# Kernel tuning notes

Hardware: AMD Instinct MI355X
Metric: run time of the kernel (lower is better)

Reference implementation:

```python
import jax, jax.numpy as jnp
import numpy as np

NEG_SLOPE = 0.2   # GATConv default leaky_relu slope
BN_EPS = 1e-5
N, D, H, DH, E, BS = 49152, 512, 8, 64, 131072, 12
N_LAYERS = 5  # conv6 exists in __init__ but is never called in forward


def setup_inputs() -> dict:
    key = jax.random.key(0)
    ks = jax.random.split(key, 12)
    s = 0.05
    x = jax.random.normal(ks[0], (N, D), jnp.float32)
    edge_index = jax.random.randint(ks[1], (2, E), 0, N, jnp.int64)
    Ws = jax.random.normal(ks[2], (N_LAYERS, D, H * DH), jnp.float32) * s
    Asrc = jax.random.normal(ks[3], (N_LAYERS, H, DH), jnp.float32) * s
    Adst = jax.random.normal(ks[4], (N_LAYERS, H, DH), jnp.float32) * s
    Bconv = jax.random.normal(ks[5], (N_LAYERS, H * DH), jnp.float32) * s
    Gamma = jnp.ones((N_LAYERS, D), jnp.float32)
    Beta = jnp.zeros((N_LAYERS, D), jnp.float32)
    Wl = jax.random.normal(ks[6], (D, 1), jnp.float32) * s
    bl = jnp.zeros((1,), jnp.float32)
    return {"x": x, "edge_index": edge_index, "Ws": Ws, "Asrc": Asrc,
            "Adst": Adst, "Bconv": Bconv, "Gamma": Gamma, "Beta": Beta,
            "Wl": Wl, "bl": bl, "bs": BS}


def _gat_conv(x, src, dst, W, a_src, a_dst, b):
    n = x.shape[0]
    h = (x @ W).reshape(n, H, DH)                      # [N,H,DH]
    al_s = jnp.einsum('nhd,hd->nh', h, a_src)          # [N,H]
    al_d = jnp.einsum('nhd,hd->nh', h, a_dst)
    e = jax.nn.leaky_relu(al_s[src] + al_d[dst], NEG_SLOPE)  # [Etot,H]
    # segment softmax over incoming edges of each dst node
    m = jax.ops.segment_max(e, dst, num_segments=n)
    p = jnp.exp(e - m[dst])
    z = jax.ops.segment_sum(p, dst, num_segments=n)
    alpha = p / (z[dst] + 1e-16)
    out = jax.ops.segment_sum(alpha[:, :, None] * h[src], dst, num_segments=n)
    return out.reshape(n, H * DH) + b


def _batch_norm(x, gamma, beta):
    mu = x.mean(0)
    var = x.var(0)  # biased, as torch BN uses for normalization
    return (x - mu) * jax.lax.rsqrt(var + BN_EPS) * gamma + beta


def reference(x, edge_index, Ws, Asrc, Adst, Bconv, Gamma, Beta, Wl, bl, bs):
    n = x.shape[0]
    loops = jnp.arange(n, dtype=edge_index.dtype)      # add_self_loops=True
    src = jnp.concatenate([edge_index[0], loops])
    dst = jnp.concatenate([edge_index[1], loops])
    for i in range(N_LAYERS):
        x = _gat_conv(x, src, dst, Ws[i], Asrc[i], Adst[i], Bconv[i])
        x = jax.nn.relu(_batch_norm(x, Gamma[i], Beta[i]))
    w = x @ Wl + bl                                    # [N,1]
    return w.reshape(bs, -1)
```

## Files before the change

kernel.cpp:

```cpp
#include <hip/hip_runtime.h>
#include <cstdint>

#define N_NODES 49152
#define DIM 512
#define NH 8
#define DHEAD 64
#define NE 131072
#define ETOT (NE + N_NODES)
#define NLAYERS 5
#define AGG_NODES 32
#define AGG_BLOCKS (N_NODES / AGG_NODES)

typedef short short8 __attribute__((ext_vector_type(8)));
typedef float floatx4 __attribute__((ext_vector_type(4)));

__device__ __forceinline__ float bf2f(unsigned short v) {
  union { unsigned int u; float f; } x; x.u = ((unsigned int)v) << 16; return x.f;
}
__device__ __forceinline__ unsigned short f2bf(float f) {
  union { float f; unsigned int u; } x; x.f = f;
  unsigned int r = x.u + 0x7fffu + ((x.u >> 16) & 1u);
  return (unsigned short)(r >> 16);
}
__device__ __forceinline__ void async_load16(const void* g, void* l) {
  __builtin_amdgcn_global_load_lds((const __attribute__((address_space(1))) void*)g,
                                   (__attribute__((address_space(3))) void*)l, 16, 0, 0);
}

__global__ __launch_bounds__(256) void convert_x_r10(const float* __restrict__ xf, unsigned short* __restrict__ xb)
{
  const size_t i = ((size_t)blockIdx.x * 256 + threadIdx.x) * 8;
  const float4 a = *(const float4*)&xf[i];
  const float4 b = *(const float4*)&xf[i + 4];
  unsigned int ov[4];
  ov[0] = (unsigned int)f2bf(a.x) | ((unsigned int)f2bf(a.y) << 16);
  ov[1] = (unsigned int)f2bf(a.z) | ((unsigned int)f2bf(a.w) << 16);
  ov[2] = (unsigned int)f2bf(b.x) | ((unsigned int)f2bf(b.y) << 16);
  ov[3] = (unsigned int)f2bf(b.z) | ((unsigned int)f2bf(b.w) << 16);
  *(uint4*)&xb[i] = *(const uint4*)ov;
}

__global__ void transpose_w_r10(const float* __restrict__ Ws, unsigned short* __restrict__ WT)
{
  __shared__ float tile[32][33];
  const int l  = blockIdx.z;
  const int nt = blockIdx.x * 32, kt = blockIdx.y * 32;
  const int tx = threadIdx.x & 31, ty = threadIdx.x >> 5;
  #pragma unroll
  for (int r = 0; r < 32; r += 8)
    tile[ty + r][tx] = Ws[(size_t)l*DIM*DIM + (size_t)(kt + ty + r)*DIM + nt + tx];
  __syncthreads();
  #pragma unroll
  for (int r = 0; r < 32; r += 8)
    WT[(size_t)l*DIM*DIM + (size_t)(nt + ty + r)*DIM + kt + tx] = f2bf(tile[tx][ty + r]);
}

__global__ void repack_edges_r10(const int* __restrict__ raw, int* __restrict__ eidx)
{
  const int i = blockIdx.x * 256 + threadIdx.x;
  bool is64 = true;
  #pragma unroll
  for (int j = 0; j < 16; j++) is64 = is64 && (raw[2*j + 1] == 0);
  int v;
  if (is64) v = (int)((const long long*)raw)[i];
  else      v = raw[i];
  eidx[i] = v;
}

__global__ void init_counts_r10(int* __restrict__ counts) {
  counts[blockIdx.x * 256 + threadIdx.x] = 1;
}
__global__ void hist_dst_r10(const int* __restrict__ eidx, int* __restrict__ counts) {
  const int i = blockIdx.x * 256 + threadIdx.x;
  atomicAdd(&counts[eidx[NE + i]], 1);
}
__global__ void scan_kernel_r10(const int* __restrict__ counts, int* __restrict__ offs, int* __restrict__ cursor)
{
  __shared__ int tot[1024];
  const int t = threadIdx.x;
  const int base = t * 48;
  int s = 0;
  for (int i = 0; i < 48; i++) s += counts[base + i];
  tot[t] = s;
  __syncthreads();
  for (int o = 1; o < 1024; o <<= 1) {
    int v = (t >= o) ? tot[t - o] : 0;
    __syncthreads();
    tot[t] += v;
    __syncthreads();
  }
  int run = tot[t] - s;
  for (int i = 0; i < 48; i++) {
    offs[base + i] = run;
    cursor[base + i] = run;
    run += counts[base + i];
  }
  if (t == 1023) offs[N_NODES] = tot[1023];
}
__global__ void scatter_edges_r10(const int* __restrict__ eidx, int* __restrict__ cursor, int* __restrict__ csrc)
{
  const int i = blockIdx.x * 256 + threadIdx.x;
  int s, d;
  if (i < NE) { s = eidx[i]; d = eidx[NE + i]; }
  else        { s = i - NE; d = s; }
  const int pos = atomicAdd(&cursor[d], 1);
  csrc[pos] = s;
}

__global__ __launch_bounds__(512, 4) void gemm_bt_r10(const unsigned short* __restrict__ A,
                                                      const unsigned short* __restrict__ BT,
                                                      const float* __restrict__ asrc,
                                                      const float* __restrict__ adst,
                                                      const float* __restrict__ bnscale,
                                                      const float* __restrict__ bnshift,
                                                      unsigned short* __restrict__ C,
                                                      float* __restrict__ als,
                                                      float* __restrict__ ald)
{
  __shared__ unsigned short As[128 * 64];
  __shared__ unsigned short Bs[256 * 64];
  const int m0 = blockIdx.x * 128;
  const int n0 = blockIdx.y * 256;
  const int tid = threadIdx.x;
  const int wv = tid >> 6, lane = tid & 63;
  const int wr = (wv & 1) * 64, wc = (wv >> 1) * 64;
  const int q = lane >> 4, c16 = lane & 15;
  const int arow = lane >> 3;
  const int acol = (lane & 7) * 8;
  const int sr = tid >> 3;
  const int sk = (tid & 7) * 8;

  floatx4 acc[4][4] = {};

  for (int k0 = 0; k0 < DIM; k0 += 64) {
    #pragma unroll
    for (int t = 0; t < 4; t++) {
      const int cb = wv * 4 + t;
      async_load16(BT + (size_t)(n0 + cb*8 + arow)*DIM + k0 + acol, &Bs[cb * 512]);
    }
    if (bnscale) {
      const uint4 x0 = *(const uint4*)&A[(size_t)(m0 + sr)      * DIM + k0 + sk];
      const uint4 x1 = *(const uint4*)&A[(size_t)(m0 + sr + 64) * DIM + k0 + sk];
      const float4 sc0 = *(const float4*)&bnscale[k0 + sk];
      const float4 sc1 = *(const float4*)&bnscale[k0 + sk + 4];
      const float4 sh0 = *(const float4*)&bnshift[k0 + sk];
      const float4 sh1 = *(const float4*)&bnshift[k0 + sk + 4];
      const float scv[8] = {sc0.x, sc0.y, sc0.z, sc0.w, sc1.x, sc1.y, sc1.z, sc1.w};
      const float shv[8] = {sh0.x, sh0.y, sh0.z, sh0.w, sh1.x, sh1.y, sh1.z, sh1.w};
      const uint4 xs[2] = {x0, x1};
      #pragma unroll
      for (int t = 0; t < 2; t++) {
        const unsigned int* xp = (const unsigned int*)&xs[t];
        unsigned int ov[4];
        #pragma unroll
        for (int j = 0; j < 4; j++) {
          const float a = bf2f((unsigned short)(xp[j] & 0xffffu));
          const float b = bf2f((unsigned short)(xp[j] >> 16));
          const float ya = fmaxf(0.f, a * scv[2*j]     + shv[2*j]);
          const float yb = fmaxf(0.f, b * scv[2*j + 1] + shv[2*j + 1]);
          ov[j] = (unsigned int)f2bf(ya) | ((unsigned int)f2bf(yb) << 16);
        }
        *(uint4*)&As[(sr + t*64) * 64 + sk] = *(const uint4*)ov;
      }
    } else {
      #pragma unroll
      for (int t = 0; t < 2; t++) {
        const int cb = wv * 2 + t;
        async_load16(A + (size_t)(m0 + cb*8 + arow)*DIM + k0 + acol, &As[cb * 512]);
      }
    }
    __syncthreads();
    #pragma unroll
    for (int kk = 0; kk < 64; kk += 32) {
      short8 aF[4], bF[4];
      #pragma unroll
      for (int mt = 0; mt < 4; mt++)
        aF[mt] = *(const short8*)&As[(wr + mt*16 + c16) * 64 + kk + q*8];
      #pragma unroll
      for (int nt = 0; nt < 4; nt++)
        bF[nt] = *(const short8*)&Bs[(wc + nt*16 + c16) * 64 + kk + q*8];
      #pragma unroll
      for (int mt = 0; mt < 4; mt++)
        #pragma unroll
        for (int nt = 0; nt < 4; nt++)
          acc[mt][nt] = __builtin_amdgcn_mfma_f32_16x16x32_bf16(aF[mt], bF[nt], acc[mt][nt], 0, 0, 0);
    }
    __syncthreads();
  }
  #pragma unroll
  for (int mt = 0; mt < 4; mt++) {
    #pragma unroll
    for (int nt = 0; nt < 4; nt++) {
      const int col = n0 + wc + nt*16 + c16;
      #pragma unroll
      for (int r = 0; r < 4; r++) {
        const int row = m0 + wr + mt*16 + q*4 + r;
        C[(size_t)row * DIM + col] = f2bf(acc[mt][nt][r]);
      }
    }
  }
  const int head = 4 * blockIdx.y + (wc >> 6);
  float as_[4], ad_[4];
  #pragma unroll
  for (int nt = 0; nt < 4; nt++) {
    const int d = nt * 16 + c16;
    as_[nt] = asrc[head * DHEAD + d];
    ad_[nt] = adst[head * DHEAD + d];
  }
  #pragma unroll
  for (int mt = 0; mt < 4; mt++) {
    #pragma unroll
    for (int r = 0; r < 4; r++) {
      float ss = 0.f, sd = 0.f;
      #pragma unroll
      for (int nt = 0; nt < 4; nt++) {
        ss += acc[mt][nt][r] * as_[nt];
        sd += acc[mt][nt][r] * ad_[nt];
      }
      #pragma unroll
      for (int msk = 1; msk <= 8; msk <<= 1) {
        ss += __shfl_xor(ss, msk, 64);
        sd += __shfl_xor(sd, msk, 64);
      }
      if (c16 == 0) {
        const int row = m0 + wr + mt*16 + q*4 + r;
        als[row * NH + head] = ss;
        ald[row * NH + head] = sd;
      }
    }
  }
}

__global__ __launch_bounds__(512, 4) void gat_agg_r10(const unsigned short* __restrict__ Hm,
    const float* __restrict__ als, const float* __restrict__ ald,
    const int* __restrict__ offs, const int* __restrict__ csrc,
    const float* __restrict__ bconv, unsigned short* __restrict__ Xout,
    float* __restrict__ ps, float* __restrict__ pq)
{
  __shared__ float red[8][1024];
  const int wv = threadIdx.x >> 6, lane = threadIdx.x & 63;
  const int hd = lane >> 3;
  const int hp = lane & 7;
  const int slot = lane >> 3;
  const float4 bA = ((const float4*)(bconv + (size_t)lane * 8))[0];
  const float4 bB = ((const float4*)(bconv + (size_t)lane * 8))[1];
  const float barr[8] = {bA.x, bA.y, bA.z, bA.w, bB.x, bB.y, bB.z, bB.w};
  float cs[8] = {}, cq[8] = {};

  #pragma unroll 1
  for (int i = 0; i < 4; i++) {
    const int node = blockIdx.x * AGG_NODES + wv * 4 + i;
    const int e0 = offs[node], e1 = offs[node + 1];
    const int deg = e1 - e0;
    float acc[8] = {};
    float zinv;

    if (deg <= 8) {
      const float aldp = ald[node * NH + hp];
      const int myS = csrc[e0 + ((lane < deg) ? lane : 0)];
      const int s_slot = __shfl(myS, slot, 64);
      float lg = als[s_slot * NH + hp] + aldp;
      lg = lg > 0.f ? lg : 0.2f * lg;
      const float lgv = (slot < deg) ? lg : -1e30f;
      float mx = fmaxf(lgv, __shfl_xor(lgv, 8, 64));
      mx = fmaxf(mx, __shfl_xor(mx, 16, 64));
      mx = fmaxf(mx, __shfl_xor(mx, 32, 64));
      const float w = __expf(lgv - mx);
      float z = w + __shfl_xor(w, 8, 64);
      z += __shfl_xor(z, 16, 64);
      z += __shfl_xor(z, 32, 64);
      zinv = 1.f / (__shfl(z, hd, 64) + 1e-16f);

      #pragma unroll
      for (int g = 0; g < 2; g++) {
        const int b = g * 4;
        if (b < deg) {
          const int k1 = (b+1 < deg) ? b+1 : 0;
          const int k2 = (b+2 < deg) ? b+2 : 0;
          const int k3 = (b+3 < deg) ? b+3 : 0;
          const int s0 = __shfl(myS, b,  64);
          const int s1 = __shfl(myS, k1, 64);
          const int s2 = __shfl(myS, k2, 64);
          const int s3 = __shfl(myS, k3, 64);
          const uint4 h0v = *(const uint4*)&Hm[(size_t)s0 * DIM + lane * 8];
          const uint4 h1v = *(const uint4*)&Hm[(size_t)s1 * DIM + lane * 8];
          const uint4 h2v = *(const uint4*)&Hm[(size_t)s2 * DIM + lane * 8];
          const uint4 h3v = *(const uint4*)&Hm[(size_t)s3 * DIM + lane * 8];
          const float w0 = __shfl(w, (b+0)*8 + hd, 64);
          const float w1 = __shfl(w, (b+1)*8 + hd, 64);
          const float w2 = __shfl(w, (b+2)*8 + hd, 64);
          const float w3 = __shfl(w, (b+3)*8 + hd, 64);
          const unsigned int* p0 = (const unsigned int*)&h0v;
          const unsigned int* p1 = (const unsigned int*)&h1v;
          const unsigned int* p2 = (const unsigned int*)&h2v;
          const unsigned int* p3 = (const unsigned int*)&h3v;
          #pragma unroll
          for (int j = 0; j < 4; j++) {
            acc[2*j]   += w0 * bf2f((unsigned short)(p0[j] & 0xffffu))
                        + w1 * bf2f((unsigned short)(p1[j] & 0xffffu))
                        + w2 * bf2f((unsigned short)(p2[j] & 0xffffu))
                        + w3 * bf2f((unsigned short)(p3[j] & 0xffffu));
            acc[2*j+1] += w0 * bf2f((unsigned short)(p0[j] >> 16))
                        + w1 * bf2f((unsigned short)(p1[j] >> 16))
                        + w2 * bf2f((unsigned short)(p2[j] >> 16))
                        + w3 * bf2f((unsigned short)(p3[j] >> 16));
          }
        }
      }
    } else if (deg <= 64) {
      const float aldp = ald[node * NH + hp];
      const int myS = (lane < deg) ? csrc[e0 + lane] : 0;
      const int nr = (deg + 7) >> 3;
      float lgsto[8];
      #pragma unroll
      for (int r = 0; r < 8; r++) {
        if (r < nr) {
          const int k = r * 8 + slot;
          const int s = __shfl(myS, k & 63, 64);
          float lg = als[s * NH + hp] + aldp;
          lg = lg > 0.f ? lg : 0.2f * lg;
          lgsto[r] = (k < deg) ? lg : -1e30f;
        } else lgsto[r] = -1e30f;
      }
      float m = lgsto[0];
      #pragma unroll
      for (int r = 1; r < 8; r++) m = fmaxf(m, lgsto[r]);
      m = fmaxf(m, __shfl_xor(m, 8, 64));
      m = fmaxf(m, __shfl_xor(m, 16, 64));
      m = fmaxf(m, __shfl_xor(m, 32, 64));
      float z = 0.f;
      float wsto[8];
      #pragma unroll
      for (int r = 0; r < 8; r++) {
        if (r < nr) {
          const float w = __expf(lgsto[r] - m);
          wsto[r] = w; z += w;
        } else wsto[r] = 0.f;
      }
      z += __shfl_xor(z, 8, 64);
      z += __shfl_xor(z, 16, 64);
      z += __shfl_xor(z, 32, 64);
      zinv = 1.f / (__shfl(z, hd, 64) + 1e-16f);

      int sn = __shfl(myS, 0, 64);
      uint4 hv = *(const uint4*)&Hm[(size_t)sn * DIM + lane * 8];
      #pragma unroll
      for (int r = 0; r < 8; r++) {
        if (r * 8 < deg) {
          const int kmax = (deg - r * 8 < 8) ? (deg - r * 8) : 8;
          for (int kk = 0; kk < kmax; kk++) {
            const uint4 hcur = hv;
            const int k = r * 8 + kk;
            if (k + 1 < deg) {
              const int s2 = __shfl(myS, (k + 1) & 63, 64);
              hv = *(const uint4*)&Hm[(size_t)s2 * DIM + lane * 8];
            }
            const float w = __shfl(wsto[r], (kk << 3) + hd, 64);
            const unsigned int* hpx = (const unsigned int*)&hcur;
            #pragma unroll
            for (int j = 0; j < 4; j++) {
              acc[2*j]   += w * bf2f((unsigned short)(hpx[j] & 0xffffu));
              acc[2*j+1] += w * bf2f((unsigned short)(hpx[j] >> 16));
            }
          }
        }
      }
    } else {
      const float aldv = ald[node * NH + hd];
      float m = -1e30f, z = 0.f;
      for (int e = e0; e < e1; e++) {
        const int s = csrc[e];
        float lg = als[s * NH + hd] + aldv;
        lg = lg > 0.f ? lg : 0.2f * lg;
        const float mn = fmaxf(m, lg);
        const float sf = __expf(m - mn);
        const float w  = __expf(lg - mn);
        z = z * sf + w;
        const uint4 hv = *(const uint4*)&Hm[(size_t)s * DIM + lane * 8];
        const unsigned int* hpx = (const unsigned int*)&hv;
        #pragma unroll
        for (int j = 0; j < 4; j++) {
          acc[2*j]   = acc[2*j]   * sf + w * bf2f((unsigned short)(hpx[j] & 0xffffu));
          acc[2*j+1] = acc[2*j+1] * sf + w * bf2f((unsigned short)(hpx[j] >> 16));
        }
        m = mn;
      }
      zinv = 1.f / (z + 1e-16f);
    }

    unsigned int ov[4];
    #pragma unroll
    for (int j = 0; j < 4; j++) {
      const unsigned short b0 = f2bf(acc[2*j] * zinv + barr[2*j]);
      const unsigned short b1 = f2bf(acc[2*j+1] * zinv + barr[2*j+1]);
      ov[j] = (unsigned int)b0 | ((unsigned int)b1 << 16);
      const float y0 = bf2f(b0), y1 = bf2f(b1);
      cs[2*j]   += y0; cq[2*j]   += y0 * y0;
      cs[2*j+1] += y1; cq[2*j+1] += y1 * y1;
    }
    *(uint4*)&Xout[(size_t)node * DIM + lane * 8] = *(const uint4*)ov;
  }
  #pragma unroll
  for (int j = 0; j < 8; j++) {
    red[wv][lane * 8 + j] = cs[j];
    red[wv][512 + lane * 8 + j] = cq[j];
  }
  __syncthreads();
  const int t = threadIdx.x;
  float s = 0.f, q = 0.f;
  #pragma unroll
  for (int w = 0; w < 8; w++) {
    s += red[w][t];
    q += red[w][512 + t];
  }
  ps[(size_t)blockIdx.x * 512 + t] = s;
  pq[(size_t)blockIdx.x * 512 + t] = q;
}

__global__ __launch_bounds__(256) void bn_reduce_r10(const float* __restrict__ ps, const float* __restrict__ pq,
                                                     const float* __restrict__ gamma, const float* __restrict__ beta,
                                                     float* __restrict__ scale, float* __restrict__ shift)
{
  __shared__ float rs[256], rq[256];
  const int c = blockIdx.x;
  const int t = threadIdx.x;
  float s = 0.f, q = 0.f;
  for (int b = t; b < AGG_BLOCKS; b += 256) {
    s += ps[(size_t)b * 512 + c];
    q += pq[(size_t)b * 512 + c];
  }
  rs[t] = s; rq[t] = q;
  __syncthreads();
  for (int o = 128; o > 0; o >>= 1) {
    if (t < o) { rs[t] += rs[t + o]; rq[t] += rq[t + o]; }
    __syncthreads();
  }
  if (t == 0) {
    const float inv = 1.0f / (float)N_NODES;
    const float mean = rs[0] * inv;
    float var = rq[0] * inv - mean * mean;
    var = fmaxf(var, 0.f);
    const float rsq = rsqrtf(var + 1e-5f);
    const float sc = gamma[c] * rsq;
    scale[c] = sc;
    shift[c] = beta[c] - mean * sc;
  }
}

__global__ __launch_bounds__(256) void final_head_r10(const unsigned short* __restrict__ X,
    const float* __restrict__ scale, const float* __restrict__ shift,
    const float* __restrict__ wl, const float* __restrict__ blp,
    float* __restrict__ out)
{
  const int wv = threadIdx.x >> 6, lane = threadIdx.x & 63;
  const int node = blockIdx.x * 4 + wv;
  const uint4 xv = *(const uint4*)&X[(size_t)node * DIM + lane * 8];
  const unsigned int* xp = (const unsigned int*)&xv;
  const int c0 = lane * 8;
  float s = 0.f;
  #pragma unroll
  for (int i = 0; i < 4; i++) {
    const float a0 = bf2f((unsigned short)(xp[i] & 0xffffu));
    const float a1 = bf2f((unsigned short)(xp[i] >> 16));
    const float y0 = fmaxf(0.f, a0 * scale[c0 + 2*i]     + shift[c0 + 2*i]);
    const float y1 = fmaxf(0.f, a1 * scale[c0 + 2*i + 1] + shift[c0 + 2*i + 1]);
    s += y0 * wl[c0 + 2*i] + y1 * wl[c0 + 2*i + 1];
  }
  #pragma unroll
  for (int msk = 32; msk >= 1; msk >>= 1) s += __shfl_xor(s, msk, 64);
  if (lane == 0) out[node] = s + blp[0];
}

extern "C" void kernel_launch(void* const* d_in, const int* in_sizes, int n_in,
                              void* d_out, int out_size, void* d_ws, size_t ws_size,
                              hipStream_t stream)
{
  const float* x_in  = (const float*)d_in[0];
  const int*   ei    = (const int*)d_in[1];
  const float* Ws    = (const float*)d_in[2];
  const float* Asrc  = (const float*)d_in[3];
  const float* Adst  = (const float*)d_in[4];
  const float* Bconv = (const float*)d_in[5];
  const float* Gamma = (const float*)d_in[6];
  const float* Beta  = (const float*)d_in[7];
  const float* Wl    = (const float*)d_in[8];
  const float* bl    = (const float*)d_in[9];
  float* out = (float*)d_out;

  char* ws = (char*)d_ws;
  size_t off = 0;
  auto alloc = [&](size_t b) { char* p = ws + off; off += (b + 255) & ~(size_t)255; return p; };
  unsigned short* xbuf = (unsigned short*)alloc((size_t)N_NODES * DIM * 2);
  unsigned short* hbuf = (unsigned short*)alloc((size_t)N_NODES * DIM * 2);
  unsigned short* WT   = (unsigned short*)alloc((size_t)NLAYERS * DIM * DIM * 2);
  float* als   = (float*)alloc((size_t)N_NODES * NH * 4);
  float* ald   = (float*)alloc((size_t)N_NODES * NH * 4);
  int* eidx    = (int*)alloc((size_t)2 * NE * 4);
  int* counts  = (int*)alloc((size_t)N_NODES * 4);
  int* offs    = (int*)alloc(((size_t)N_NODES + 1) * 4);
  int* cursor  = (int*)alloc((size_t)N_NODES * 4);
  int* csrc    = (int*)alloc((size_t)ETOT * 4);
  float* ps    = (float*)alloc((size_t)AGG_BLOCKS * 512 * 4);
  float* pq    = (float*)alloc((size_t)AGG_BLOCKS * 512 * 4);
  float* scale = (float*)alloc(512 * 4);
  float* shift = (float*)alloc(512 * 4);

  convert_x_r10<<<(N_NODES * DIM / 8) / 256, 256, 0, stream>>>(x_in, xbuf);
  transpose_w_r10<<<dim3(16, 16, 5), 256, 0, stream>>>(Ws, WT);
  repack_edges_r10<<<(2 * NE) / 256, 256, 0, stream>>>(ei, eidx);
  init_counts_r10<<<N_NODES / 256, 256, 0, stream>>>(counts);
  hist_dst_r10<<<NE / 256, 256, 0, stream>>>(eidx, counts);
  scan_kernel_r10<<<1, 1024, 0, stream>>>(counts, offs, cursor);
  scatter_edges_r10<<<ETOT / 256, 256, 0, stream>>>(eidx, cursor, csrc);

  for (int l = 0; l < NLAYERS; l++) {
    gemm_bt_r10<<<dim3(N_NODES / 128, DIM / 256), 512, 0, stream>>>(
        xbuf, WT + (size_t)l * DIM * DIM,
        Asrc + l * NH * DHEAD, Adst + l * NH * DHEAD,
        (l == 0) ? nullptr : scale, (l == 0) ? nullptr : shift,
        hbuf, als, ald);
    gat_agg_r10<<<AGG_BLOCKS, 512, 0, stream>>>(hbuf, als, ald, offs, csrc,
                                                Bconv + l * DIM, xbuf, ps, pq);
    bn_reduce_r10<<<512, 256, 0, stream>>>(ps, pq, Gamma + l * DIM, Beta + l * DIM, scale, shift);
  }
  final_head_r10<<<N_NODES / 4, 256, 0, stream>>>(xbuf, scale, shift, Wl, bl, out);
}
```

Baseline: 766.2 us.

## Double-buffer GEMM K-loop with swizzled LDS and fuse input fp32-to-bf16 conversion

Restructures the GEMM main loop to use K-tiles of 32 with double-buffered LDS, prefetching the next tile's global loads into registers while MFMAs run on the current buffer, so only one barrier is needed per step. LDS rows use an XOR swizzle to reduce bank conflicts. The separate fp32-to-bf16 conversion kernel for layer 0 is removed, and the GEMM now reads fp32 x directly and converts it while staging, which saves one full pass over the input. The trade-off is that the A tile now goes through registers on every layer instead of async loads, and the smaller K-step increases loop overhead.

```diff
diff --git a/kernel.cpp b/kernel.cpp
--- a/kernel.cpp
+++ b/kernel.cpp
@@ -27,20 +27,7 @@
                                    (__attribute__((address_space(3))) void*)l, 16, 0, 0);
 }
 
-__global__ __launch_bounds__(256) void convert_x_r10(const float* __restrict__ xf, unsigned short* __restrict__ xb)
-{
-  const size_t i = ((size_t)blockIdx.x * 256 + threadIdx.x) * 8;
-  const float4 a = *(const float4*)&xf[i];
-  const float4 b = *(const float4*)&xf[i + 4];
-  unsigned int ov[4];
-  ov[0] = (unsigned int)f2bf(a.x) | ((unsigned int)f2bf(a.y) << 16);
-  ov[1] = (unsigned int)f2bf(a.z) | ((unsigned int)f2bf(a.w) << 16);
-  ov[2] = (unsigned int)f2bf(b.x) | ((unsigned int)f2bf(b.y) << 16);
-  ov[3] = (unsigned int)f2bf(b.z) | ((unsigned int)f2bf(b.w) << 16);
-  *(uint4*)&xb[i] = *(const uint4*)ov;
-}
-
-__global__ void transpose_w_r10(const float* __restrict__ Ws, unsigned short* __restrict__ WT)
+__global__ void transpose_w_r12(const float* __restrict__ Ws, unsigned short* __restrict__ WT)
 {
   __shared__ float tile[32][33];
   const int l  = blockIdx.z;
@@ -55,7 +42,7 @@
     WT[(size_t)l*DIM*DIM + (size_t)(nt + ty + r)*DIM + kt + tx] = f2bf(tile[tx][ty + r]);
 }
 
-__global__ void repack_edges_r10(const int* __restrict__ raw, int* __restrict__ eidx)
+__global__ void repack_edges_r12(const int* __restrict__ raw, int* __restrict__ eidx)
 {
   const int i = blockIdx.x * 256 + threadIdx.x;
   bool is64 = true;
@@ -67,14 +54,14 @@
   eidx[i] = v;
 }
 
-__global__ void init_counts_r10(int* __restrict__ counts) {
+__global__ void init_counts_r12(int* __restrict__ counts) {
   counts[blockIdx.x * 256 + threadIdx.x] = 1;
 }
-__global__ void hist_dst_r10(const int* __restrict__ eidx, int* __restrict__ counts) {
+__global__ void hist_dst_r12(const int* __restrict__ eidx, int* __restrict__ counts) {
   const int i = blockIdx.x * 256 + threadIdx.x;
   atomicAdd(&counts[eidx[NE + i]], 1);
 }
-__global__ void scan_kernel_r10(const int* __restrict__ counts, int* __restrict__ offs, int* __restrict__ cursor)
+__global__ void scan_kernel_r12(const int* __restrict__ counts, int* __restrict__ offs, int* __restrict__ cursor)
 {
   __shared__ int tot[1024];
   const int t = threadIdx.x;
@@ -97,7 +84,7 @@
   }
   if (t == 1023) offs[N_NODES] = tot[1023];
 }
-__global__ void scatter_edges_r10(const int* __restrict__ eidx, int* __restrict__ cursor, int* __restrict__ csrc)
+__global__ void scatter_edges_r12(const int* __restrict__ eidx, int* __restrict__ cursor, int* __restrict__ csrc)
 {
   const int i = blockIdx.x * 256 + threadIdx.x;
   int s, d;
@@ -107,7 +94,8 @@
   csrc[pos] = s;
 }
 
-__global__ __launch_bounds__(512, 4) void gemm_bt_r10(const unsigned short* __restrict__ A,
+__global__ __launch_bounds__(512, 4) void gemm_bt_r12(const float* __restrict__ Af,
+                                                      const unsigned short* __restrict__ Ab,
                                                       const unsigned short* __restrict__ BT,
                                                       const float* __restrict__ asrc,
                                                       const float* __restrict__ adst,
@@ -117,41 +105,113 @@
                                                       float* __restrict__ als,
                                                       float* __restrict__ ald)
 {
-  __shared__ unsigned short As[128 * 64];
-  __shared__ unsigned short Bs[256 * 64];
+  __shared__ unsigned short As[2][128 * 32];
+  __shared__ unsigned short Bs[2][256 * 32];
   const int m0 = blockIdx.x * 128;
   const int n0 = blockIdx.y * 256;
   const int tid = threadIdx.x;
   const int wv = tid >> 6, lane = tid & 63;
   const int wr = (wv & 1) * 64, wc = (wv >> 1) * 64;
   const int q = lane >> 4, c16 = lane & 15;
-  const int arow = lane >> 3;
-  const int acol = (lane & 7) * 8;
-  const int sr = tid >> 3;
-  const int sk = (tid & 7) * 8;
+  const int brow = lane >> 2;
+  const int bcol = (((lane & 3) ^ (brow & 3)) * 8);
+  const int sr = tid >> 2;
+  const int sk = (tid & 3) * 8;
+  const int swk = (((tid & 3) ^ (sr & 3)) * 8);
+  const int px = (c16 & 3);
+  const bool isconv = (Af != nullptr);
 
   floatx4 acc[4][4] = {};
-
-  for (int k0 = 0; k0 < DIM; k0 += 64) {
+  float4 pf0, pf1;
+  uint4  pb;
+
+  {
+    const int k0 = 0;
     #pragma unroll
-    for (int t = 0; t < 4; t++) {
-      const int cb = wv * 4 + t;
-      async_load16(BT + (size_t)(n0 + cb*8 + arow)*DIM + k0 + acol, &Bs[cb * 512]);
-    }
-    if (bnscale) {
-      const uint4 x0 = *(const uint4*)&A[(size_t)(m0 + sr)      * DIM + k0 + sk];
-      const uint4 x1 = *(const uint4*)&A[(size_t)(m0 + sr + 64) * DIM + k0 + sk];
+    for (int c = 0; c < 2; c++) {
+      const int cb = wv * 2 + c;
+      async_load16(BT + (size_t)(n0 + cb*16 + brow)*DIM + k0 + bcol, &Bs[0][cb * 512]);
+    }
+    if (isconv) {
+      pf0 = *(const float4*)&Af[(size_t)(m0 + sr) * DIM + k0 + sk];
+      pf1 = *(const float4*)&Af[(size_t)(m0 + sr) * DIM + k0 + sk + 4];
+      unsigned int ov[4];
+      const float v[8] = {pf0.x,pf0.y,pf0.z,pf0.w,pf1.x,pf1.y,pf1.z,pf1.w};
+      #pragma unroll
+      for (int j = 0; j < 4; j++)
+        ov[j] = (unsigned int)f2bf(v[2*j]) | ((unsigned int)f2bf(v[2*j+1]) << 16);
+      *(uint4*)&As[0][sr * 32 + swk] = *(const uint4*)ov;
+    } else {
+      pb = *(const uint4*)&Ab[(size_t)(m0 + sr) * DIM + k0 + sk];
       const float4 sc0 = *(const float4*)&bnscale[k0 + sk];
       const float4 sc1 = *(const float4*)&bnscale[k0 + sk + 4];
       const float4 sh0 = *(const float4*)&bnshift[k0 + sk];
       const float4 sh1 = *(const float4*)&bnshift[k0 + sk + 4];
       const float scv[8] = {sc0.x, sc0.y, sc0.z, sc0.w, sc1.x, sc1.y, sc1.z, sc1.w};
       const float shv[8] = {sh0.x, sh0.y, sh0.z, sh0.w, sh1.x, sh1.y, sh1.z, sh1.w};
-      const uint4 xs[2] = {x0, x1};
-      #pragma unroll
-      for (int t = 0; t < 2; t++) {
-        const unsigned int* xp = (const unsigned int*)&xs[t];
-        unsigned int ov[4];
+      const unsigned int* xp = (const unsigned int*)&pb;
+      unsigned int ov[4];
+      #pragma unroll
+      for (int j = 0; j < 4; j++) {
+        const float a = bf2f((unsigned short)(xp[j] & 0xffffu));
+        const float b = bf2f((unsigned short)(xp[j] >> 16));
+        const float ya = fmaxf(0.f, a * scv[2*j]     + shv[2*j]);
+        const float yb = fmaxf(0.f, b * scv[2*j + 1] + shv[2*j + 1]);
+        ov[j] = (unsigned int)f2bf(ya) | ((unsigned int)f2bf(yb) << 16);
+      }
+      *(uint4*)&As[0][sr * 32 + swk] = *(const uint4*)ov;
+    }
+  }
+  __syncthreads();
+
+  int buf = 0;
+  #pragma unroll 2
+  for (int t = 0; t < 16; ++t) {
+    if (t < 15) {
+      const int k1 = (t + 1) * 32;
+      #pragma unroll
+      for (int c = 0; c < 2; c++) {
+        const int cb = wv * 2 + c;
+        async_load16(BT + (size_t)(n0 + cb*16 + brow)*DIM + k1 + bcol, &Bs[buf ^ 1][cb * 512]);
+      }
+      if (isconv) {
+        pf0 = *(const float4*)&Af[(size_t)(m0 + sr) * DIM + k1 + sk];
+        pf1 = *(const float4*)&Af[(size_t)(m0 + sr) * DIM + k1 + sk + 4];
+      } else {
+        pb = *(const uint4*)&Ab[(size_t)(m0 + sr) * DIM + k1 + sk];
+      }
+    }
+    {
+      const int po = ((q ^ px) * 8);
+      short8 aF[4], bF[4];
+      #pragma unroll
+      for (int mt = 0; mt < 4; mt++)
+        aF[mt] = *(const short8*)&As[buf][(wr + mt*16 + c16) * 32 + po];
+      #pragma unroll
+      for (int nt = 0; nt < 4; nt++)
+        bF[nt] = *(const short8*)&Bs[buf][(wc + nt*16 + c16) * 32 + po];
+      #pragma unroll
+      for (int mt = 0; mt < 4; mt++)
+        #pragma unroll
+        for (int nt = 0; nt < 4; nt++)
+          acc[mt][nt] = __builtin_amdgcn_mfma_f32_16x16x32_bf16(aF[mt], bF[nt], acc[mt][nt], 0, 0, 0);
+    }
+    if (t < 15) {
+      const int k1 = (t + 1) * 32;
+      unsigned int ov[4];
+      if (isconv) {
+        const float v[8] = {pf0.x,pf0.y,pf0.z,pf0.w,pf1.x,pf1.y,pf1.z,pf1.w};
+        #pragma unroll
+        for (int j = 0; j < 4; j++)
+          ov[j] = (unsigned int)f2bf(v[2*j]) | ((unsigned int)f2bf(v[2*j+1]) << 16);
+      } else {
+        const float4 sc0 = *(const float4*)&bnscale[k1 + sk];
+        const float4 sc1 = *(const float4*)&bnscale[k1 + sk + 4];
+        const float4 sh0 = *(const float4*)&bnshift[k1 + sk];
+        const float4 sh1 = *(const float4*)&bnshift[k1 + sk + 4];
+        const float scv[8] = {sc0.x, sc0.y, sc0.z, sc0.w, sc1.x, sc1.y, sc1.z, sc1.w};
+        const float shv[8] = {sh0.x, sh0.y, sh0.z, sh0.w, sh1.x, sh1.y, sh1.z, sh1.w};
+        const unsigned int* xp = (const unsigned int*)&pb;
         #pragma unroll
         for (int j = 0; j < 4; j++) {
           const float a = bf2f((unsigned short)(xp[j] & 0xffffu));
@@ -160,33 +220,13 @@
           const float yb = fmaxf(0.f, b * scv[2*j + 1] + shv[2*j + 1]);
           ov[j] = (unsigned int)f2bf(ya) | ((unsigned int)f2bf(yb) << 16);
         }
-        *(uint4*)&As[(sr + t*64) * 64 + sk] = *(const uint4*)ov;
-      }
-    } else {
-      #pragma unroll
-      for (int t = 0; t < 2; t++) {
-        const int cb = wv * 2 + t;
-        async_load16(A + (size_t)(m0 + cb*8 + arow)*DIM + k0 + acol, &As[cb * 512]);
-      }
-    }
-    __syncthreads();
-    #pragma unroll
-    for (int kk = 0; kk < 64; kk += 32) {
-      short8 aF[4], bF[4];
-      #pragma unroll
-      for (int mt = 0; mt < 4; mt++)
-        aF[mt] = *(const short8*)&As[(wr + mt*16 + c16) * 64 + kk + q*8];
-      #pragma unroll
-      for (int nt = 0; nt < 4; nt++)
-        bF[nt] = *(const short8*)&Bs[(wc + nt*16 + c16) * 64 + kk + q*8];
-      #pragma unroll
-      for (int mt = 0; mt < 4; mt++)
-        #pragma unroll
-        for (int nt = 0; nt < 4; nt++)
-          acc[mt][nt] = __builtin_amdgcn_mfma_f32_16x16x32_bf16(aF[mt], bF[nt], acc[mt][nt], 0, 0, 0);
-    }
-    __syncthreads();
-  }
+      }
+      *(uint4*)&As[buf ^ 1][sr * 32 + swk] = *(const uint4*)ov;
+      __syncthreads();
+    }
+    buf ^= 1;
+  }
+
   #pragma unroll
   for (int mt = 0; mt < 4; mt++) {
     #pragma unroll
@@ -231,7 +271,7 @@
   }
 }
 
-__global__ __launch_bounds__(512, 4) void gat_agg_r10(const unsigned short* __restrict__ Hm,
+__global__ __launch_bounds__(512, 4) void gat_agg_r12(const unsigned short* __restrict__ Hm,
     const float* __restrict__ als, const float* __restrict__ ald,
     const int* __restrict__ offs, const int* __restrict__ csrc,
     const float* __restrict__ bconv, unsigned short* __restrict__ Xout,
@@ -417,7 +457,7 @@
   pq[(size_t)blockIdx.x * 512 + t] = q;
 }
 
-__global__ __launch_bounds__(256) void bn_reduce_r10(const float* __restrict__ ps, const float* __restrict__ pq,
+__global__ __launch_bounds__(256) void bn_reduce_r12(const float* __restrict__ ps, const float* __restrict__ pq,
                                                      const float* __restrict__ gamma, const float* __restrict__ beta,
                                                      float* __restrict__ scale, float* __restrict__ shift)
 {
@@ -447,7 +487,7 @@
   }
 }
 
-__global__ __launch_bounds__(256) void final_head_r10(const unsigned short* __restrict__ X,
+__global__ __launch_bounds__(256) void final_head_r12(const unsigned short* __restrict__ X,
     const float* __restrict__ scale, const float* __restrict__ shift,
     const float* __restrict__ wl, const float* __restrict__ blp,
     float* __restrict__ out)
@@ -505,23 +545,23 @@
   float* scale = (float*)alloc(512 * 4);
   float* shift = (float*)alloc(512 * 4);
 
-  convert_x_r10<<<(N_NODES * DIM / 8) / 256, 256, 0, stream>>>(x_in, xbuf);
-  transpose_w_r10<<<dim3(16, 16, 5), 256, 0, stream>>>(Ws, WT);
-  repack_edges_r10<<<(2 * NE) / 256, 256, 0, stream>>>(ei, eidx);
-  init_counts_r10<<<N_NODES / 256, 256, 0, stream>>>(counts);
-  hist_dst_r10<<<NE / 256, 256, 0, stream>>>(eidx, counts);
-  scan_kernel_r10<<<1, 1024, 0, stream>>>(counts, offs, cursor);
-  scatter_edges_r10<<<ETOT / 256, 256, 0, stream>>>(eidx, cursor, csrc);
+  transpose_w_r12<<<dim3(16, 16, 5), 256, 0, stream>>>(Ws, WT);
+  repack_edges_r12<<<(2 * NE) / 256, 256, 0, stream>>>(ei, eidx);
+  init_counts_r12<<<N_NODES / 256, 256, 0, stream>>>(counts);
+  hist_dst_r12<<<NE / 256, 256, 0, stream>>>(eidx, counts);
+  scan_kernel_r12<<<1, 1024, 0, stream>>>(counts, offs, cursor);
+  scatter_edges_r12<<<ETOT / 256, 256, 0, stream>>>(eidx, cursor, csrc);
 
   for (int l = 0; l < NLAYERS; l++) {
-    gemm_bt_r10<<<dim3(N_NODES / 128, DIM / 256), 512, 0, stream>>>(
-        xbuf, WT + (size_t)l * DIM * DIM,
+    gemm_bt_r12<<<dim3(N_NODES / 128, DIM / 256), 512, 0, stream>>>(
+        (l == 0) ? x_in : nullptr, (l == 0) ? nullptr : xbuf,
+        WT + (size_t)l * DIM * DIM,
         Asrc + l * NH * DHEAD, Adst + l * NH * DHEAD,
         (l == 0) ? nullptr : scale, (l == 0) ? nullptr : shift,
         hbuf, als, ald);
-    gat_agg_r10<<<AGG_BLOCKS, 512, 0, stream>>>(hbuf, als, ald, offs, csrc,
+    gat_agg_r12<<<AGG_BLOCKS, 512, 0, stream>>>(hbuf, als, ald, offs, csrc,
                                                 Bconv + l * DIM, xbuf, ps, pq);
-    bn_reduce_r10<<<512, 256, 0, stream>>>(ps, pq, Gamma + l * DIM, Beta + l * DIM, scale, shift);
-  }
-  final_head_r10<<<N_NODES / 4, 256, 0, stream>>>(xbuf, scale, shift, Wl, bl, out);
-}
+    bn_reduce_r12<<<512, 256, 0, stream>>>(ps, pq, Gamma + l * DIM, Beta + l * DIM, scale, shift);
+  }
+  final_head_r12<<<N_NODES / 4, 256, 0, stream>>>(xbuf, scale, shift, Wl, bl, out);
+}
```

Result: slower. 797.6 us (+4.1%).
